# Performance work log

Measured on AMD Instinct MI355X. Metric: run time of the kernel, lower is better.

The kernel has to match this reference:

```python
import jax, jax.numpy as jnp
import numpy as np

TEMPERATURE = 0.07
N, D, NUM_CLASSES = 8192, 1024, 128


def setup_inputs() -> dict:
    key = jax.random.key(0)
    k1, k2 = jax.random.split(key)
    embeddings = jax.random.normal(k1, (N, D), dtype=jnp.float32)
    labels = jax.random.randint(k2, (N,), 0, NUM_CLASSES, dtype=jnp.int64)
    return {"embeddings": embeddings, "labels": labels}


def reference(embeddings, labels):
    # L2-normalize rows (eps matches F.normalize default clamp of 1e-12 on the norm)
    norm = jnp.maximum(jnp.linalg.norm(embeddings, axis=-1, keepdims=True), 1e-12)
    emb = embeddings / norm
    # [N, N] similarity scaled by temperature
    sim = jnp.matmul(emb, emb.T) / TEMPERATURE
    # positive mask: same label, diagonal zeroed
    pos_mask = (labels[:, None] == labels[None, :]).astype(sim.dtype)
    pos_mask = pos_mask * (1.0 - jnp.eye(sim.shape[0], dtype=sim.dtype))
    exp_sim = jnp.exp(sim)
    sum_exp = exp_sim.sum(axis=1)              # [N]
    pos_sum = (exp_sim * pos_mask).sum(axis=1)  # [N]
    loss = -jnp.log(pos_sum / sum_exp)
    return loss.mean()
```

## Files before the change

### kernel.cpp

```cpp
#include <hip/hip_runtime.h>
#include <hip/hip_bf16.h>
#include <math.h>

#define N 8192
#define D 1024
#define TILE 128
#define BK 64
#define NTILES (N / TILE)
#define NBLOCKS (NTILES * (NTILES + 1) / 2)

typedef __bf16 bf16_t;
typedef bf16_t bf16x4 __attribute__((ext_vector_type(4)));
typedef bf16_t bf16x8 __attribute__((ext_vector_type(8)));
typedef float f32x4 __attribute__((ext_vector_type(4)));

#define POST_SCALE 4.5398124f

__global__ __launch_bounds__(256) void norm_cast(const float* __restrict__ in,
                                                 bf16_t* __restrict__ out,
                                                 float* __restrict__ sums) {
    const int row = blockIdx.x;
    const int tid = threadIdx.x;
    if (row < 64) sums[row * 256 + tid] = 0.f;
    const float4 v = ((const float4*)(in + (size_t)row * D))[tid];
    float ss = v.x * v.x + v.y * v.y + v.z * v.z + v.w * v.w;
    #pragma unroll
    for (int off = 32; off >= 1; off >>= 1) ss += __shfl_xor(ss, off, 64);
    __shared__ float red[4];
    const int wave = tid >> 6, lane = tid & 63;
    if (lane == 0) red[wave] = ss;
    __syncthreads();
    const float tot = red[0] + red[1] + red[2] + red[3];
    const float scale = POST_SCALE / fmaxf(sqrtf(tot), 1e-12f);
    bf16x4 o;
    o[0] = (bf16_t)(v.x * scale);
    o[1] = (bf16_t)(v.y * scale);
    o[2] = (bf16_t)(v.z * scale);
    o[3] = (bf16_t)(v.w * scale);
    ((bf16x4*)(out + (size_t)row * D))[tid] = o;
}

__global__ __launch_bounds__(256, 4) void gemm_fused(
        const bf16_t* __restrict__ E, const int* __restrict__ labels,
        float* __restrict__ sumExp, float* __restrict__ posSum) {
    __shared__ char smem[2 * TILE * BK * 2];
    __shared__ int labR[TILE], labC[TILE];

    const int b = blockIdx.x;
    int ti = (int)((sqrtf(8.0f * (float)b + 1.0f) - 1.0f) * 0.5f);
    while ((ti + 1) * (ti + 2) / 2 <= b) ++ti;
    while (ti * (ti + 1) / 2 > b) --ti;
    const int tj = b - ti * (ti + 1) / 2;
    const bool isDiag = (ti == tj);

    const int tid     = threadIdx.x;
    const int wave    = tid >> 6;
    const int lane    = tid & 63;
    const int q       = lane >> 4;
    const int lr      = lane & 15;
    const int waveRow = wave >> 1;
    const int waveCol = wave & 1;
    const int rowStart = ti * TILE;
    const int colStart = tj * TILE;

    if (tid < TILE) labR[tid] = labels[rowStart + tid];
    else            labC[tid - TILE] = labels[colStart + (tid - TILE)];

    f32x4 acc[4][4];
    #pragma unroll
    for (int i = 0; i < 4; ++i)
        #pragma unroll
        for (int j = 0; j < 4; ++j)
            acc[i][j] = {0.f, 0.f, 0.f, 0.f};

    const int   srow = wave * 8 + (lane >> 3);
    const int   uc   = (lane & 7) ^ (lane >> 3);
    const char* gaBase = (const char*)(E + (size_t)rowStart * D) + srow * (D * 2) + uc * 16;
    const char* gbBase = (const char*)(E + (size_t)colStart * D) + srow * (D * 2) + uc * 16;

    unsigned aAddr[2], bAddr[2];
    #pragma unroll
    for (int h = 0; h < 2; ++h) {
        const unsigned un = (unsigned)((h * 4 + q) ^ (lr & 7));
        aAddr[h] = (unsigned)((waveRow * 64 + lr) * 128) + un * 16;
        bAddr[h] = (unsigned)(16384 + (waveCol * 64 + lr) * 128) + un * 16;
    }

    for (int it = 0; it < 16; ++it) {
        const unsigned kb = (unsigned)it * 128;
        #pragma unroll
        for (int p = 0; p < 4; ++p) {
            const char* ga = gaBase + kb + p * (32 * D * 2);
            const char* gb = gbBase + kb + p * (32 * D * 2);
            char* la = smem + (p * 256 + wave * 64) * 16;
            char* lb = smem + 16384 + (p * 256 + wave * 64) * 16;
            __builtin_amdgcn_global_load_lds(
                (const __attribute__((address_space(1))) void*)ga,
                (__attribute__((address_space(3))) void*)la, 16, 0, 0);
            __builtin_amdgcn_global_load_lds(
                (const __attribute__((address_space(1))) void*)gb,
                (__attribute__((address_space(3))) void*)lb, 16, 0, 0);
        }
        __syncthreads();

        #pragma unroll
        for (int h = 0; h < 2; ++h) {
            bf16x8 af[4], bfr[4];
            #pragma unroll
            for (int ri = 0; ri < 4; ++ri)
                af[ri] = *(const bf16x8*)(smem + aAddr[h] + ri * 2048);
            #pragma unroll
            for (int ci = 0; ci < 4; ++ci)
                bfr[ci] = *(const bf16x8*)(smem + bAddr[h] + ci * 2048);
            #pragma unroll
            for (int ri = 0; ri < 4; ++ri)
                #pragma unroll
                for (int ci = 0; ci < 4; ++ci)
                    acc[ri][ci] = __builtin_amdgcn_mfma_f32_16x16x32_bf16(
                        af[ri], bfr[ci], acc[ri][ci], 0, 0, 0);
        }
        __syncthreads();
    }

    float colAll[4] = {0.f, 0.f, 0.f, 0.f};
    float colPos[4] = {0.f, 0.f, 0.f, 0.f};
    #pragma unroll
    for (int ri = 0; ri < 4; ++ri) {
        #pragma unroll
        for (int e = 0; e < 4; ++e) {
            const int rloc = waveRow * 64 + ri * 16 + q * 4 + e;
            const int gi   = rowStart + rloc;
            const int li   = labR[rloc];
            float s_all = 0.f, s_pos = 0.f;
            #pragma unroll
            for (int ci = 0; ci < 4; ++ci) {
                const int cloc = waveCol * 64 + ci * 16 + lr;
                const int gj   = colStart + cloc;
#if __has_builtin(__builtin_amdgcn_exp2f)
                const float v = __builtin_amdgcn_exp2f(acc[ri][ci][e]);
#else
                const float v = exp2f(acc[ri][ci][e]);
#endif
                const bool same = (labC[cloc] == li);
                const float vp  = same ? v : 0.f;
                s_all += v;
                if (gi != gj) s_pos += vp;
                if (!isDiag) {
                    colAll[ci] += v;
                    colPos[ci] += vp;
                }
            }
            #pragma unroll
            for (int off = 1; off < 16; off <<= 1) {
                s_all += __shfl_xor(s_all, off, 64);
                s_pos += __shfl_xor(s_pos, off, 64);
            }
            if (lr == 0) {
                atomicAdd(&sumExp[gi], s_all);
                atomicAdd(&posSum[gi], s_pos);
            }
        }
    }
    if (!isDiag) {
        #pragma unroll
        for (int ci = 0; ci < 4; ++ci) {
            float a = colAll[ci], p = colPos[ci];
            a += __shfl_xor(a, 16, 64);  a += __shfl_xor(a, 32, 64);
            p += __shfl_xor(p, 16, 64);  p += __shfl_xor(p, 32, 64);
            if (q == 0) {
                const int gj = colStart + waveCol * 64 + ci * 16 + lr;
                atomicAdd(&sumExp[gj], a);
                atomicAdd(&posSum[gj], p);
            }
        }
    }
}

__global__ __launch_bounds__(1024) void finalize(const float* __restrict__ sumExp,
                                                 const float* __restrict__ posSum,
                                                 float* __restrict__ out) {
    const int tid = threadIdx.x;
    float s = 0.f;
    #pragma unroll
    for (int i = tid; i < N; i += 1024)
        s += __logf(sumExp[i] / posSum[i]);
    #pragma unroll
    for (int off = 32; off >= 1; off >>= 1) s += __shfl_xor(s, off, 64);
    __shared__ float red[16];
    if ((tid & 63) == 0) red[tid >> 6] = s;
    __syncthreads();
    if (tid == 0) {
        float t = 0.f;
        #pragma unroll
        for (int i = 0; i < 16; ++i) t += red[i];
        out[0] = t / (float)N;
    }
}

extern "C" void kernel_launch(void* const* d_in, const int* in_sizes, int n_in,
                              void* d_out, int out_size, void* d_ws, size_t ws_size,
                              hipStream_t stream) {
    const float* emb    = (const float*)d_in[0];
    const int*   labels = (const int*)d_in[1];
    float* out = (float*)d_out;

    float*  sumExp = (float*)d_ws;
    float*  posSum = sumExp + N;
    bf16_t* EN     = (bf16_t*)((char*)d_ws + (size_t)2 * N * sizeof(float));

    norm_cast<<<N, 256, 0, stream>>>(emb, EN, sumExp);

    gemm_fused<<<NBLOCKS, 256, 0, stream>>>(EN, labels, sumExp, posSum);

    finalize<<<1, 1024, 0, stream>>>(sumExp, posSum, out);
}
```

Baseline: 228.1 us.

## Switch similarity GEMM from bf16 to fp8 scaled MFMA

Result: slower. 583.3 us (+155.7%).

```diff
diff --git a/kernel.cpp b/kernel.cpp
--- a/kernel.cpp
+++ b/kernel.cpp
@@ -5,19 +5,17 @@
 #define N 8192
 #define D 1024
 #define TILE 128
-#define BK 64
 #define NTILES (N / TILE)
 #define NBLOCKS (NTILES * (NTILES + 1) / 2)
 
-typedef __bf16 bf16_t;
-typedef bf16_t bf16x4 __attribute__((ext_vector_type(4)));
-typedef bf16_t bf16x8 __attribute__((ext_vector_type(8)));
 typedef float f32x4 __attribute__((ext_vector_type(4)));
+typedef int   i32x4 __attribute__((ext_vector_type(4)));
+typedef int   i32x8 __attribute__((ext_vector_type(8)));
 
 #define POST_SCALE 4.5398124f
 
 __global__ __launch_bounds__(256) void norm_cast(const float* __restrict__ in,
-                                                 bf16_t* __restrict__ out,
+                                                 unsigned char* __restrict__ out,
                                                  float* __restrict__ sums) {
     const int row = blockIdx.x;
     const int tid = threadIdx.x;
@@ -32,18 +30,15 @@
     __syncthreads();
     const float tot = red[0] + red[1] + red[2] + red[3];
     const float scale = POST_SCALE / fmaxf(sqrtf(tot), 1e-12f);
-    bf16x4 o;
-    o[0] = (bf16_t)(v.x * scale);
-    o[1] = (bf16_t)(v.y * scale);
-    o[2] = (bf16_t)(v.z * scale);
-    o[3] = (bf16_t)(v.w * scale);
-    ((bf16x4*)(out + (size_t)row * D))[tid] = o;
+    int w = __builtin_amdgcn_cvt_pk_fp8_f32(v.x * scale, v.y * scale, 0, false);
+    w = __builtin_amdgcn_cvt_pk_fp8_f32(v.z * scale, v.w * scale, w, true);
+    ((int*)(out + (size_t)row * D))[tid] = w;
 }
 
 __global__ __launch_bounds__(256, 4) void gemm_fused(
-        const bf16_t* __restrict__ E, const int* __restrict__ labels,
+        const unsigned char* __restrict__ E, const int* __restrict__ labels,
         float* __restrict__ sumExp, float* __restrict__ posSum) {
-    __shared__ char smem[2 * TILE * BK * 2];
+    __shared__ unsigned char smem[2 * TILE * 128];
     __shared__ int labR[TILE], labC[TILE];
 
     const int b = blockIdx.x;
@@ -73,27 +68,24 @@
         for (int j = 0; j < 4; ++j)
             acc[i][j] = {0.f, 0.f, 0.f, 0.f};
 
-    const int   srow = wave * 8 + (lane >> 3);
-    const int   uc   = (lane & 7) ^ (lane >> 3);
-    const char* gaBase = (const char*)(E + (size_t)rowStart * D) + srow * (D * 2) + uc * 16;
-    const char* gbBase = (const char*)(E + (size_t)colStart * D) + srow * (D * 2) + uc * 16;
-
-    unsigned aAddr[2], bAddr[2];
-    #pragma unroll
-    for (int h = 0; h < 2; ++h) {
-        const unsigned un = (unsigned)((h * 4 + q) ^ (lr & 7));
-        aAddr[h] = (unsigned)((waveRow * 64 + lr) * 128) + un * 16;
-        bAddr[h] = (unsigned)(16384 + (waveCol * 64 + lr) * 128) + un * 16;
-    }
-
-    for (int it = 0; it < 16; ++it) {
+    const int r0 = tid >> 3;
+    const int lc = (tid & 7) ^ (r0 & 7);
+    const unsigned char* gaBase = E + (size_t)(rowStart + r0) * D + lc * 16;
+    const unsigned char* gbBase = E + (size_t)(colStart + r0) * D + lc * 16;
+
+    const unsigned x     = (unsigned)(lr & 7);
+    const unsigned aBase = (unsigned)((waveRow * 64 + lr) * 128);
+    const unsigned bBase = (unsigned)(16384 + (waveCol * 64 + lr) * 128);
+    const unsigned u0    = ((2u * q) ^ x) * 16;
+
+    for (int it = 0; it < 8; ++it) {
         const unsigned kb = (unsigned)it * 128;
         #pragma unroll
         for (int p = 0; p < 4; ++p) {
-            const char* ga = gaBase + kb + p * (32 * D * 2);
-            const char* gb = gbBase + kb + p * (32 * D * 2);
-            char* la = smem + (p * 256 + wave * 64) * 16;
-            char* lb = smem + 16384 + (p * 256 + wave * 64) * 16;
+            const unsigned char* ga = gaBase + kb + p * 32 * D;
+            const unsigned char* gb = gbBase + kb + p * 32 * D;
+            char* la = (char*)smem + (p * 256 + wave * 64) * 16;
+            char* lb = (char*)smem + 16384 + (p * 256 + wave * 64) * 16;
             __builtin_amdgcn_global_load_lds(
                 (const __attribute__((address_space(1))) void*)ga,
                 (__attribute__((address_space(3))) void*)la, 16, 0, 0);
@@ -103,21 +95,23 @@
         }
         __syncthreads();
 
-        #pragma unroll
-        for (int h = 0; h < 2; ++h) {
-            bf16x8 af[4], bfr[4];
+        i32x8 af[4];
+        #pragma unroll
+        for (int ri = 0; ri < 4; ++ri) {
+            const i32x4 lo = *(const i32x4*)(smem + aBase + ri * 2048 + u0);
+            const i32x4 hi = *(const i32x4*)(smem + aBase + ri * 2048 + (u0 ^ 16));
+            af[ri] = __builtin_shufflevector(lo, hi, 0, 1, 2, 3, 4, 5, 6, 7);
+        }
+        #pragma unroll
+        for (int ci = 0; ci < 4; ++ci) {
+            const i32x4 lo = *(const i32x4*)(smem + bBase + ci * 2048 + u0);
+            const i32x4 hi = *(const i32x4*)(smem + bBase + ci * 2048 + (u0 ^ 16));
+            const i32x8 bf = __builtin_shufflevector(lo, hi, 0, 1, 2, 3, 4, 5, 6, 7);
             #pragma unroll
             for (int ri = 0; ri < 4; ++ri)
-                af[ri] = *(const bf16x8*)(smem + aAddr[h] + ri * 2048);
-            #pragma unroll
-            for (int ci = 0; ci < 4; ++ci)
-                bfr[ci] = *(const bf16x8*)(smem + bAddr[h] + ci * 2048);
-            #pragma unroll
-            for (int ri = 0; ri < 4; ++ri)
-                #pragma unroll
-                for (int ci = 0; ci < 4; ++ci)
-                    acc[ri][ci] = __builtin_amdgcn_mfma_f32_16x16x32_bf16(
-                        af[ri], bfr[ci], acc[ri][ci], 0, 0, 0);
+                acc[ri][ci] = __builtin_amdgcn_mfma_scale_f32_16x16x128_f8f6f4(
+                    af[ri], bf, acc[ri][ci], 0, 0,
+                    0, 0x7F7F7F7F, 0, 0x7F7F7F7F);
         }
         __syncthreads();
     }
@@ -204,9 +198,9 @@
     const int*   labels = (const int*)d_in[1];
     float* out = (float*)d_out;
 
-    float*  sumExp = (float*)d_ws;
-    float*  posSum = sumExp + N;
-    bf16_t* EN     = (bf16_t*)((char*)d_ws + (size_t)2 * N * sizeof(float));
+    float*         sumExp = (float*)d_ws;
+    float*         posSum = sumExp + N;
+    unsigned char* EN     = (unsigned char*)((char*)d_ws + (size_t)2 * N * sizeof(float));
 
     norm_cast<<<N, 256, 0, stream>>>(emb, EN, sumExp);
 
```
